# Optimization experiments

Hardware: AMD Instinct MI355X
Metric: run time of the kernel (lower is better)

The kernel has to match this reference:

```python
import jax, jax.numpy as jnp
import numpy as np

N, E, G = 40000, 640000, 64
IN, H, OUT = 128, 256, 128


def setup_inputs() -> dict:
    key = jax.random.key(0)
    ks = jax.random.split(key, 8)
    x = jax.random.normal(ks[0], (N, IN), dtype=jnp.float32)
    edge_index = jax.random.randint(ks[1], (2, E), 0, N, dtype=jnp.int64)
    batch = jnp.sort(jax.random.randint(ks[2], (N,), 0, G, dtype=jnp.int64))
    glorot = lambda k, sh: jax.random.normal(k, sh, jnp.float32) * (1.0 / np.sqrt(sh[0]))
    return {
        "x": x,
        "edge_index": edge_index,
        "batch": batch,
        "W_in": glorot(ks[3], (IN, H)), "b_in": jnp.zeros((H,), jnp.float32),
        "W_mid": glorot(ks[4], (H, H)), "b_mid": jnp.zeros((H,), jnp.float32),
        "W_out": glorot(ks[5], (H, OUT)), "b_out": jnp.zeros((OUT,), jnp.float32),
        "W_cls": glorot(ks[6], (OUT, 2)), "b_cls": jnp.zeros((2,), jnp.float32),
    }


def _gcn_conv(x, src, dst, deg_inv_sqrt, W, b):
    # PyG GCNConv: h = x @ W; propagate with symmetric norm (self-loops added); + bias
    h = x @ W
    norm = deg_inv_sqrt[src] * deg_inv_sqrt[dst]            # [E]
    agg = jax.ops.segment_sum(norm[:, None] * h[src], dst, num_segments=x.shape[0])
    agg = agg + (deg_inv_sqrt * deg_inv_sqrt)[:, None] * h  # self-loop contribution
    return agg + b


def reference(x, edge_index, batch, W_in, b_in, W_mid, b_mid, W_out, b_out, W_cls, b_cls):
    src, dst = edge_index[0], edge_index[1]
    n = x.shape[0]
    # degree with self-loops (in-degree on dst, matching PyG default flow)
    deg = jax.ops.segment_sum(jnp.ones((src.shape[0],), x.dtype), dst, num_segments=n) + 1.0
    dis = jax.lax.rsqrt(deg)

    h = jax.nn.relu(_gcn_conv(x, src, dst, dis, W_in, b_in))
    h = jax.nn.relu(_gcn_conv(h, src, dst, dis, W_mid, b_mid))   # num_layers - 2 = 1 middle layer
    node_embeddings = _gcn_conv(h, src, dst, dis, W_out, b_out)

    # global mean pool over graphs
    counts = jax.ops.segment_sum(jnp.ones((n,), x.dtype), batch, num_segments=G)
    graph_embedding = jax.ops.segment_sum(node_embeddings, batch, num_segments=G) / jnp.maximum(counts, 1.0)[:, None]

    logits = graph_embedding @ W_cls + b_cls
    return (node_embeddings, graph_embedding, logits)
```

## Files before the change

### kernel.cpp

```cpp
#include <hip/hip_runtime.h>
#include <hip/hip_bf16.h>

#define Nn   40000
#define Ee   640000
#define Gg   64
#define INF  128
#define Hh   256
#define OUTF 128

#define NBLK_N 157

typedef _Float16 half8 __attribute__((ext_vector_type(8)));
typedef float    f32x4 __attribute__((ext_vector_type(4)));

__global__ __launch_bounds__(256) void k_count(const int* __restrict__ dst, int* __restrict__ cnt) {
    int e = blockIdx.x * 256 + threadIdx.x;
    if (e < Ee) atomicAdd(&cnt[dst[e]], 1);
}

__global__ __launch_bounds__(256)
void k_scan1(int* __restrict__ cnt, int* __restrict__ offs, int* __restrict__ partial,
             float* __restrict__ dis) {
    __shared__ int sm[256];
    int i = blockIdx.x * 256 + threadIdx.x;
    int v = 0;
    if (i < Nn) {
        v = cnt[i];
        dis[i] = rsqrtf((float)v + 1.0f);
        cnt[i] = 0;
    }
    sm[threadIdx.x] = v;
    __syncthreads();
#pragma unroll
    for (int d = 1; d < 256; d <<= 1) {
        int t = (threadIdx.x >= d) ? sm[threadIdx.x - d] : 0;
        __syncthreads();
        sm[threadIdx.x] += t;
        __syncthreads();
    }
    if (i < Nn) offs[i] = sm[threadIdx.x] - v;
    if (threadIdx.x == 255) partial[blockIdx.x] = sm[255];
}

__global__ __launch_bounds__(256)
void k_scan2(int* __restrict__ partial) {
    __shared__ int sm[256];
    int v = (threadIdx.x < NBLK_N) ? partial[threadIdx.x] : 0;
    sm[threadIdx.x] = v;
    __syncthreads();
#pragma unroll
    for (int d = 1; d < 256; d <<= 1) {
        int t = (threadIdx.x >= d) ? sm[threadIdx.x - d] : 0;
        __syncthreads();
        sm[threadIdx.x] += t;
        __syncthreads();
    }
    if (threadIdx.x < NBLK_N) partial[threadIdx.x] = sm[threadIdx.x] - v;
}

__global__ __launch_bounds__(256)
void k_scan3(int* __restrict__ offs, const int* __restrict__ partial) {
    int i = blockIdx.x * 256 + threadIdx.x;
    if (i < Nn) offs[i] += partial[blockIdx.x];
    if (i == 0) offs[Nn] = Ee;
}

__global__ __launch_bounds__(256)
void k_fill(const int* __restrict__ src, const int* __restrict__ dst,
            const int* __restrict__ offs, int* __restrict__ cursor,
            unsigned short* __restrict__ src_sorted) {
    int e = blockIdx.x * 256 + threadIdx.x;
    if (e >= Ee) return;
    int d = dst[e];
    int pos = offs[d] + atomicAdd(&cursor[d], 1);
    src_sorted[pos] = (unsigned short)src[e];
}

__global__ __launch_bounds__(256)
void k_cvt_all(const float* __restrict__ x, const float* __restrict__ dis,
               _Float16* __restrict__ xs,
               const float* __restrict__ W_in,  _Float16* __restrict__ Wt_in,
               const float* __restrict__ W_mid, _Float16* __restrict__ Wt_mid,
               const float* __restrict__ W_out, _Float16* __restrict__ Wt_out,
               float* __restrict__ ge_accum) {
    int bid = blockIdx.x;
    int tid = threadIdx.x;
    if (bid < 5000) {
        int i = (bid * 256 + tid) * 4;
        float s = dis[i >> 7];
        float4 v = *(const float4*)&x[i];
        xs[i + 0] = (_Float16)(s * v.x);
        xs[i + 1] = (_Float16)(s * v.y);
        xs[i + 2] = (_Float16)(s * v.z);
        xs[i + 3] = (_Float16)(s * v.w);
    } else if (bid < 5128) {
        int idx = (bid - 5000) * 256 + tid;
        int n = idx >> 7, k = idx & 127;
        Wt_in[idx] = (_Float16)W_in[(size_t)k * Hh + n];
    } else if (bid < 5384) {
        int idx = (bid - 5128) * 256 + tid;
        int n = idx >> 8, k = idx & 255;
        Wt_mid[idx] = (_Float16)W_mid[(size_t)k * Hh + n];
    } else if (bid < 5512) {
        int idx = (bid - 5384) * 256 + tid;
        int n = idx >> 8, k = idx & 255;
        Wt_out[idx] = (_Float16)W_out[(size_t)k * OUTF + n];
    } else {
        int idx = (bid - 5512) * 256 + tid;
        ge_accum[idx] = 0.0f;
    }
}

template <bool BR>
__global__ __launch_bounds__(256)
void k_gemm_mfma(const _Float16* __restrict__ A, const _Float16* __restrict__ Wt,
                 const float* __restrict__ dis, const float* __restrict__ bias,
                 _Float16* __restrict__ C16, int M, int N, int K) {
    __shared__ _Float16 Alds[128 * 40];
    __shared__ _Float16 Blds[128 * 40];
    const int tid = threadIdx.x;
    const int lane = tid & 63;
    const int waveId = tid >> 6;
    const int waveRow = waveId >> 1;
    const int waveCol = waveId & 1;
    const int quad = lane >> 4;
    const int m16 = lane & 15;
    const int rowBase = blockIdx.x * 128;
    const int colBase = blockIdx.y * 128;

    const int sRow  = tid >> 1;
    const int sKoff = (tid & 1) * 16;

    int gr = rowBase + sRow; if (gr >= M) gr = M - 1;
    const int gn = colBase + sRow;

    f32x4 acc[4][4];
#pragma unroll
    for (int i = 0; i < 4; ++i)
#pragma unroll
        for (int j = 0; j < 4; ++j)
            acc[i][j] = (f32x4){0.0f, 0.0f, 0.0f, 0.0f};

    for (int k0 = 0; k0 < K; k0 += 32) {
        const uint4* ap = (const uint4*)(A  + (size_t)gr * K + k0 + sKoff);
        const uint4* bp = (const uint4*)(Wt + (size_t)gn * K + k0 + sKoff);
        uint4 a0 = ap[0], a1 = ap[1];
        uint4 b0 = bp[0], b1 = bp[1];
        __syncthreads();
        *(uint4*)&Alds[sRow * 40 + sKoff]     = a0;
        *(uint4*)&Alds[sRow * 40 + sKoff + 8] = a1;
        *(uint4*)&Blds[sRow * 40 + sKoff]     = b0;
        *(uint4*)&Blds[sRow * 40 + sKoff + 8] = b1;
        __syncthreads();

        half8 a_frag[4], b_frag[4];
#pragma unroll
        for (int rt = 0; rt < 4; ++rt)
            a_frag[rt] = *(const half8*)&Alds[(waveRow * 64 + rt * 16 + m16) * 40 + quad * 8];
#pragma unroll
        for (int ct = 0; ct < 4; ++ct)
            b_frag[ct] = *(const half8*)&Blds[(waveCol * 64 + ct * 16 + m16) * 40 + quad * 8];
#pragma unroll
        for (int rt = 0; rt < 4; ++rt)
#pragma unroll
            for (int ct = 0; ct < 4; ++ct)
                acc[rt][ct] = __builtin_amdgcn_mfma_f32_16x16x32_f16(
                    a_frag[rt], b_frag[ct], acc[rt][ct], 0, 0, 0);
    }

#pragma unroll
    for (int rt = 0; rt < 4; ++rt) {
        const int rb = rowBase + waveRow * 64 + rt * 16 + quad * 4;
#pragma unroll
        for (int r = 0; r < 4; ++r) {
            const int row = rb + r;
            if (row < M) {
                const float s = dis[row];
#pragma unroll
                for (int ct = 0; ct < 4; ++ct) {
                    const int col = colBase + waveCol * 64 + ct * 16 + m16;
                    float v = acc[rt][ct][r];
                    if constexpr (BR) {
                        v = fmaxf(v + bias[col], 0.0f);
                    } else {
                        v = s * v;
                    }
                    C16[(size_t)row * N + col] = (_Float16)v;
                }
            }
        }
    }
}

template <int HH, bool RELU, bool H16OUT, bool HASBIAS>
__global__ __launch_bounds__(256)
void k_gatherh(const int* __restrict__ offs, const unsigned short* __restrict__ srcs,
               const float* __restrict__ dis, const _Float16* __restrict__ hp,
               const float* __restrict__ bias, void* __restrict__ outv) {
    constexpr int V = HH / 64;
    typedef _Float16 halfv __attribute__((ext_vector_type(V)));
    int n = blockIdx.x * 4 + (threadIdx.x >> 6);
    if (n >= Nn) return;
    int lane = threadIdx.x & 63;
    int col = lane * V;
    int b = __builtin_amdgcn_readfirstlane(offs[n]);
    int e = __builtin_amdgcn_readfirstlane(offs[n + 1]);

    float acc[V];
    {
        halfv sv = *(const halfv*)(hp + (size_t)n * HH + col);
#pragma unroll
        for (int j = 0; j < V; ++j) acc[j] = (float)sv[j];
    }

    int i = b;
    for (; i + 4 <= e; i += 4) {
        int s0 = srcs[i], s1 = srcs[i + 1], s2 = srcs[i + 2], s3 = srcs[i + 3];
        halfv v0 = *(const halfv*)(hp + (size_t)s0 * HH + col);
        halfv v1 = *(const halfv*)(hp + (size_t)s1 * HH + col);
        halfv v2 = *(const halfv*)(hp + (size_t)s2 * HH + col);
        halfv v3 = *(const halfv*)(hp + (size_t)s3 * HH + col);
#pragma unroll
        for (int j = 0; j < V; ++j)
            acc[j] += (float)v0[j] + (float)v1[j] + (float)v2[j] + (float)v3[j];
    }
    for (; i < e; ++i) {
        int s0 = srcs[i];
        halfv v0 = *(const halfv*)(hp + (size_t)s0 * HH + col);
#pragma unroll
        for (int j = 0; j < V; ++j) acc[j] += (float)v0[j];
    }

    float dn = dis[n];
    float r[V];
#pragma unroll
    for (int j = 0; j < V; ++j) {
        r[j] = dn * acc[j];
        if (HASBIAS) r[j] += bias[col + j];
        if (RELU) r[j] = fmaxf(r[j], 0.0f);
    }
    if constexpr (H16OUT) {
        halfv hv;
#pragma unroll
        for (int j = 0; j < V; ++j) hv[j] = (_Float16)r[j];
        *(halfv*)((_Float16*)outv + (size_t)n * HH + col) = hv;
    } else {
        if constexpr (V == 4) {
            *(float4*)((float*)outv + (size_t)n * HH + col) = make_float4(r[0], r[1], r[2], r[3]);
        } else {
            *(float2*)((float*)outv + (size_t)n * HH + col) = make_float2(r[0], r[1]);
        }
    }
}

__global__ __launch_bounds__(256)
void k_pool_accum(const float* __restrict__ emb, const int* __restrict__ batch,
                  float* __restrict__ ge_accum) {
    int n0 = blockIdx.x * 64;
    int nend = min(n0 + 64, Nn);
    int sub = threadIdx.x >> 6;
    int col = (threadIdx.x & 63) * 2;
    float ax = 0.0f, ay = 0.0f;
    int cur_g = -1;
    for (int n = n0 + sub; n < nend; n += 4) {
        int g = batch[n];
        if (g != cur_g) {
            if (cur_g >= 0) {
                unsafeAtomicAdd(&ge_accum[cur_g * OUTF + col], ax);
                unsafeAtomicAdd(&ge_accum[cur_g * OUTF + col + 1], ay);
            }
            cur_g = g; ax = 0.0f; ay = 0.0f;
        }
        float2 v = *(const float2*)&emb[(size_t)n * OUTF + col];
        ax += v.x; ay += v.y;
    }
    if (cur_g >= 0) {
        unsafeAtomicAdd(&ge_accum[cur_g * OUTF + col], ax);
        unsafeAtomicAdd(&ge_accum[cur_g * OUTF + col + 1], ay);
    }
}

__global__ __launch_bounds__(256)
void k_pool_fin(const float* __restrict__ ge_accum, const int* __restrict__ batch,
                const float* __restrict__ Wc, const float* __restrict__ bc,
                float* __restrict__ ge_out, float* __restrict__ lg_out) {
    __shared__ float ge_s[Gg * OUTF];
    __shared__ int seg[Gg + 1];
    int t = threadIdx.x;
    if (t <= Gg) {
        int lo = 0, hi = Nn;
        while (lo < hi) { int mid = (lo + hi) >> 1; if (batch[mid] < t) lo = mid + 1; else hi = mid; }
        seg[t] = lo;
    }
    __syncthreads();
    for (int idx = t; idx < Gg * OUTF; idx += 256) {
        int g = idx >> 7;
        float cnt = (float)(seg[g + 1] - seg[g]);
        float v = ge_accum[idx] / fmaxf(cnt, 1.0f);
        ge_s[idx] = v;
        ge_out[idx] = v;
    }
    __syncthreads();
    if (t < 128) {
        int g = t >> 1, c = t & 1;
        float s = bc[c];
        for (int k = 0; k < 128; ++k) s += ge_s[g * 128 + k] * Wc[k * 2 + c];
        lg_out[t] = s;
    }
}

extern "C" void kernel_launch(void* const* d_in, const int* in_sizes, int n_in,
                              void* d_out, int out_size, void* d_ws, size_t ws_size,
                              hipStream_t stream) {
    const float* x     = (const float*)d_in[0];
    const int*   ei    = (const int*)d_in[1];
    const int*   batch = (const int*)d_in[2];
    const float* W_in  = (const float*)d_in[3];
    const float* b_in  = (const float*)d_in[4];
    const float* W_mid = (const float*)d_in[5];
    const float* b_mid = (const float*)d_in[6];
    const float* W_out = (const float*)d_in[7];
    const float* b_out = (const float*)d_in[8];
    const float* W_cls = (const float*)d_in[9];
    const float* b_cls = (const float*)d_in[10];

    const int* src = ei;
    const int* dst = ei + Ee;

    float* ws = (float*)d_ws;
    float* dis      = ws;
    int*   cnt      = (int*)(ws + 40000);
    int*   offs     = (int*)(ws + 80000);
    int*   partial  = (int*)(ws + 120064);
    float* ge_accum = ws + 120256;
    unsigned short* src_sorted = (unsigned short*)(ws + 128448);
    _Float16* xs     = (_Float16*)(ws + 448448);
    _Float16* g1     = (_Float16*)(ws + 3008448);
    _Float16* Wt_in  = (_Float16*)(ws + 5568448);
    _Float16* Wt_mid = (_Float16*)(ws + 5584832);
    _Float16* Wt_out = (_Float16*)(ws + 5617600);
    _Float16* hA     = (_Float16*)(ws + 5633984);
    _Float16* actA   = (_Float16*)(ws + 10753984);

    float* out    = (float*)d_out;
    float* ge_out = out + (size_t)Nn * OUTF;
    float* lg_out = ge_out + Gg * OUTF;

    const int nBlkE = (Ee + 255) / 256;
    const int gRows = (Nn + 127) / 128;
    const int nBlkG = (Nn + 3) / 4;

    (void)hipMemsetAsync(cnt, 0, Nn * sizeof(int), stream);
    k_count<<<nBlkE, 256, 0, stream>>>(dst, cnt);
    k_scan1<<<NBLK_N, 256, 0, stream>>>(cnt, offs, partial, dis);
    k_scan2<<<1, 256, 0, stream>>>(partial);
    k_scan3<<<NBLK_N, 256, 0, stream>>>(offs, partial);
    k_fill<<<nBlkE, 256, 0, stream>>>(src, dst, offs, cnt, src_sorted);

    k_cvt_all<<<5544, 256, 0, stream>>>(x, dis, xs, W_in, Wt_in, W_mid, Wt_mid, W_out, Wt_out, ge_accum);

    k_gatherh<INF, false, true, false><<<nBlkG, 256, 0, stream>>>(offs, src_sorted, dis, xs, nullptr, g1);
    k_gemm_mfma<true><<<dim3(gRows, Hh / 128), 256, 0, stream>>>(g1, Wt_in, dis, b_in, actA, Nn, Hh, INF);

    k_gemm_mfma<false><<<dim3(gRows, Hh / 128), 256, 0, stream>>>(actA, Wt_mid, dis, nullptr, hA, Nn, Hh, Hh);
    k_gatherh<Hh, true, true, true><<<nBlkG, 256, 0, stream>>>(offs, src_sorted, dis, hA, b_mid, actA);

    k_gemm_mfma<false><<<dim3(gRows, OUTF / 128), 256, 0, stream>>>(actA, Wt_out, dis, nullptr, hA, Nn, OUTF, Hh);
    k_gatherh<OUTF, false, false, true><<<nBlkG, 256, 0, stream>>>(offs, src_sorted, dis, hA, b_out, out);

    k_pool_accum<<<(Nn + 63) / 64, 256, 0, stream>>>(out, batch, ge_accum);
    k_pool_fin<<<1, 256, 0, stream>>>(ge_accum, batch, W_cls, b_cls, ge_out, lg_out);
}
```

Baseline: 331.2 us.

## Record per-edge rank in count pass and fuse scan stages with conversion kernel

The counting kernel now stores each edge's atomic return value as a 16-bit rank, so the fill kernel places edges without a second round of atomics and the counter no longer needs resetting. The second and third scan stages are merged into the conversion kernel: each of the first 157 blocks redundantly scans the block partials and adds its own base, and the remaining blocks do the existing fp16 conversions. This removes two kernel launches and a pass of contended atomics, at the cost of extra workspace for the rank array and redundant small scans per block.

```diff
diff --git a/kernel.cpp b/kernel.cpp
--- a/kernel.cpp
+++ b/kernel.cpp
@@ -13,13 +13,15 @@
 typedef _Float16 half8 __attribute__((ext_vector_type(8)));
 typedef float    f32x4 __attribute__((ext_vector_type(4)));
 
-__global__ __launch_bounds__(256) void k_count(const int* __restrict__ dst, int* __restrict__ cnt) {
+__global__ __launch_bounds__(256)
+void k_count(const int* __restrict__ dst, int* __restrict__ cnt,
+             unsigned short* __restrict__ rank16) {
     int e = blockIdx.x * 256 + threadIdx.x;
-    if (e < Ee) atomicAdd(&cnt[dst[e]], 1);
-}
-
-__global__ __launch_bounds__(256)
-void k_scan1(int* __restrict__ cnt, int* __restrict__ offs, int* __restrict__ partial,
+    if (e < Ee) rank16[e] = (unsigned short)atomicAdd(&cnt[dst[e]], 1);
+}
+
+__global__ __launch_bounds__(256)
+void k_scan1(const int* __restrict__ cnt, int* __restrict__ offs, int* __restrict__ partial,
              float* __restrict__ dis) {
     __shared__ int sm[256];
     int i = blockIdx.x * 256 + threadIdx.x;
@@ -27,7 +29,6 @@
     if (i < Nn) {
         v = cnt[i];
         dis[i] = rsqrtf((float)v + 1.0f);
-        cnt[i] = 0;
     }
     sm[threadIdx.x] = v;
     __syncthreads();
@@ -43,72 +44,68 @@
 }
 
 __global__ __launch_bounds__(256)
-void k_scan2(int* __restrict__ partial) {
-    __shared__ int sm[256];
-    int v = (threadIdx.x < NBLK_N) ? partial[threadIdx.x] : 0;
-    sm[threadIdx.x] = v;
-    __syncthreads();
-#pragma unroll
-    for (int d = 1; d < 256; d <<= 1) {
-        int t = (threadIdx.x >= d) ? sm[threadIdx.x - d] : 0;
-        __syncthreads();
-        sm[threadIdx.x] += t;
-        __syncthreads();
-    }
-    if (threadIdx.x < NBLK_N) partial[threadIdx.x] = sm[threadIdx.x] - v;
-}
-
-__global__ __launch_bounds__(256)
-void k_scan3(int* __restrict__ offs, const int* __restrict__ partial) {
-    int i = blockIdx.x * 256 + threadIdx.x;
-    if (i < Nn) offs[i] += partial[blockIdx.x];
-    if (i == 0) offs[Nn] = Ee;
-}
-
-__global__ __launch_bounds__(256)
-void k_fill(const int* __restrict__ src, const int* __restrict__ dst,
-            const int* __restrict__ offs, int* __restrict__ cursor,
-            unsigned short* __restrict__ src_sorted) {
-    int e = blockIdx.x * 256 + threadIdx.x;
-    if (e >= Ee) return;
-    int d = dst[e];
-    int pos = offs[d] + atomicAdd(&cursor[d], 1);
-    src_sorted[pos] = (unsigned short)src[e];
-}
-
-__global__ __launch_bounds__(256)
-void k_cvt_all(const float* __restrict__ x, const float* __restrict__ dis,
-               _Float16* __restrict__ xs,
-               const float* __restrict__ W_in,  _Float16* __restrict__ Wt_in,
-               const float* __restrict__ W_mid, _Float16* __restrict__ Wt_mid,
-               const float* __restrict__ W_out, _Float16* __restrict__ Wt_out,
-               float* __restrict__ ge_accum) {
+void k_scanB(int* __restrict__ offs, const int* __restrict__ partial,
+             const float* __restrict__ x, const float* __restrict__ dis,
+             _Float16* __restrict__ xs,
+             const float* __restrict__ W_in,  _Float16* __restrict__ Wt_in,
+             const float* __restrict__ W_mid, _Float16* __restrict__ Wt_mid,
+             const float* __restrict__ W_out, _Float16* __restrict__ Wt_out,
+             float* __restrict__ ge_accum) {
     int bid = blockIdx.x;
     int tid = threadIdx.x;
-    if (bid < 5000) {
-        int i = (bid * 256 + tid) * 4;
+    if (bid < NBLK_N) {
+        __shared__ int sm[256];
+        int v = (tid < NBLK_N) ? partial[tid] : 0;
+        sm[tid] = v;
+        __syncthreads();
+#pragma unroll
+        for (int d = 1; d < 256; d <<= 1) {
+            int t = (tid >= d) ? sm[tid - d] : 0;
+            __syncthreads();
+            sm[tid] += t;
+            __syncthreads();
+        }
+        int base = (bid > 0) ? sm[bid - 1] : 0;
+        int i = bid * 256 + tid;
+        if (i < Nn) offs[i] += base;
+        if (i == 0) offs[Nn] = Ee;
+        return;
+    }
+    int b2 = bid - NBLK_N;
+    if (b2 < 5000) {
+        int i = (b2 * 256 + tid) * 4;
         float s = dis[i >> 7];
         float4 v = *(const float4*)&x[i];
         xs[i + 0] = (_Float16)(s * v.x);
         xs[i + 1] = (_Float16)(s * v.y);
         xs[i + 2] = (_Float16)(s * v.z);
         xs[i + 3] = (_Float16)(s * v.w);
-    } else if (bid < 5128) {
-        int idx = (bid - 5000) * 256 + tid;
+    } else if (b2 < 5128) {
+        int idx = (b2 - 5000) * 256 + tid;
         int n = idx >> 7, k = idx & 127;
         Wt_in[idx] = (_Float16)W_in[(size_t)k * Hh + n];
-    } else if (bid < 5384) {
-        int idx = (bid - 5128) * 256 + tid;
+    } else if (b2 < 5384) {
+        int idx = (b2 - 5128) * 256 + tid;
         int n = idx >> 8, k = idx & 255;
         Wt_mid[idx] = (_Float16)W_mid[(size_t)k * Hh + n];
-    } else if (bid < 5512) {
-        int idx = (bid - 5384) * 256 + tid;
+    } else if (b2 < 5512) {
+        int idx = (b2 - 5384) * 256 + tid;
         int n = idx >> 8, k = idx & 255;
         Wt_out[idx] = (_Float16)W_out[(size_t)k * OUTF + n];
     } else {
-        int idx = (bid - 5512) * 256 + tid;
+        int idx = (b2 - 5512) * 256 + tid;
         ge_accum[idx] = 0.0f;
     }
+}
+
+__global__ __launch_bounds__(256)
+void k_fill(const int* __restrict__ src, const int* __restrict__ dst,
+            const int* __restrict__ offs, const unsigned short* __restrict__ rank16,
+            unsigned short* __restrict__ src_sorted) {
+    int e = blockIdx.x * 256 + threadIdx.x;
+    if (e >= Ee) return;
+    int d = dst[e];
+    src_sorted[offs[d] + rank16[e]] = (unsigned short)src[e];
 }
 
 template <bool BR>
@@ -334,13 +331,14 @@
     int*   partial  = (int*)(ws + 120064);
     float* ge_accum = ws + 120256;
     unsigned short* src_sorted = (unsigned short*)(ws + 128448);
-    _Float16* xs     = (_Float16*)(ws + 448448);
-    _Float16* g1     = (_Float16*)(ws + 3008448);
-    _Float16* Wt_in  = (_Float16*)(ws + 5568448);
-    _Float16* Wt_mid = (_Float16*)(ws + 5584832);
-    _Float16* Wt_out = (_Float16*)(ws + 5617600);
-    _Float16* hA     = (_Float16*)(ws + 5633984);
-    _Float16* actA   = (_Float16*)(ws + 10753984);
+    unsigned short* rank16     = (unsigned short*)(ws + 448448);
+    _Float16* xs     = (_Float16*)(ws + 768448);
+    _Float16* g1     = (_Float16*)(ws + 3328448);
+    _Float16* Wt_in  = (_Float16*)(ws + 5888448);
+    _Float16* Wt_mid = (_Float16*)(ws + 5904832);
+    _Float16* Wt_out = (_Float16*)(ws + 5937600);
+    _Float16* hA     = (_Float16*)(ws + 5953984);
+    _Float16* actA   = (_Float16*)(ws + 11073984);
 
     float* out    = (float*)d_out;
     float* ge_out = out + (size_t)Nn * OUTF;
@@ -351,13 +349,11 @@
     const int nBlkG = (Nn + 3) / 4;
 
     (void)hipMemsetAsync(cnt, 0, Nn * sizeof(int), stream);
-    k_count<<<nBlkE, 256, 0, stream>>>(dst, cnt);
+    k_count<<<nBlkE, 256, 0, stream>>>(dst, cnt, rank16);
     k_scan1<<<NBLK_N, 256, 0, stream>>>(cnt, offs, partial, dis);
-    k_scan2<<<1, 256, 0, stream>>>(partial);
-    k_scan3<<<NBLK_N, 256, 0, stream>>>(offs, partial);
-    k_fill<<<nBlkE, 256, 0, stream>>>(src, dst, offs, cnt, src_sorted);
-
-    k_cvt_all<<<5544, 256, 0, stream>>>(x, dis, xs, W_in, Wt_in, W_mid, Wt_mid, W_out, Wt_out, ge_accum);
+    k_scanB<<<NBLK_N + 5544, 256, 0, stream>>>(offs, partial, x, dis, xs,
+                                               W_in, Wt_in, W_mid, Wt_mid, W_out, Wt_out, ge_accum);
+    k_fill<<<nBlkE, 256, 0, stream>>>(src, dst, offs, rank16, src_sorted);
 
     k_gatherh<INF, false, true, false><<<nBlkG, 256, 0, stream>>>(offs, src_sorted, dis, xs, nullptr, g1);
     k_gemm_mfma<true><<<dim3(gRows, Hh / 128), 256, 0, stream>>>(g1, Wt_in, dis, b_in, actA, Nn, Hh, INF);
```

Measured after the change: 307.4 us. 7.2% less time.
